# Optimization experiments

Hardware: AMD Instinct MI355X
Metric: run time of the kernel (lower is better)

The kernel has to match this reference:

```python
import jax, jax.numpy as jnp
import numpy as np

K = 16          # knn_graph k
FPS_RATIO = 0.5 # fps ratio
BN_EPS = 1e-5


def knn_idx(p, k):
    # p: [B, N, 3] -> neighbor indices [B, N, k] (loop=True: self included)
    n2 = jnp.sum(p * p, axis=-1)                                  # [B, N]
    d = n2[:, :, None] + n2[:, None, :] - 2.0 * jnp.einsum('bnc,bmc->bnm', p, p)
    _, idx = jax.lax.top_k(-d, k)                                 # smallest distances
    return idx


def gather_nbrs(x, idx):
    # x: [B, N, C], idx: [B, N, k] -> [B, N, k, C]
    return jax.vmap(lambda xb, ib: xb[ib])(x, idx)


def bn_silu(y, g, be):
    # training-mode BatchNorm over all rows (flattened) + SiLU, per PyG MLP defaults
    C = y.shape[-1]
    yf = y.reshape(-1, C)
    mu = jnp.mean(yf, axis=0)
    var = jnp.mean((yf - mu) ** 2, axis=0)
    return jax.nn.silu((y - mu) * jax.lax.rsqrt(var + BN_EPS) * g + be)


def fps_idx(p, m):
    # farthest point sampling on one cloud p: [N, 3], deterministic start at 0
    d0 = jnp.sum((p - p[0]) ** 2, axis=-1)
    def step(mind, _):
        i = jnp.argmax(mind)
        di = jnp.sum((p - p[i]) ** 2, axis=-1)
        return jnp.minimum(mind, di), i.astype(jnp.int32)
    _, idxs = jax.lax.scan(step, d0, None, length=m - 1)
    return jnp.concatenate([jnp.zeros((1,), jnp.int32), idxs])


def setup_inputs() -> dict:
    key = jax.random.key(0)
    ks = jax.random.split(key, 4)
    B, N, zdim = 16, 2048, 256
    return {
        'pos': jax.random.normal(ks[0], (B, N, 3), jnp.float32),
        'W1': jax.random.normal(ks[1], (6, 64), jnp.float32) * (1.0 / np.sqrt(6)),
        'b1': jnp.zeros((64,), jnp.float32),
        'g1': jnp.ones((64,), jnp.float32),
        'be1': jnp.zeros((64,), jnp.float32),
        'W2a': jax.random.normal(ks[2], (67, 128), jnp.float32) * (1.0 / np.sqrt(67)),
        'b2a': jnp.zeros((128,), jnp.float32),
        'g2a': jnp.ones((128,), jnp.float32),
        'be2a': jnp.zeros((128,), jnp.float32),
        'W2b': jax.random.normal(ks[3], (128, zdim), jnp.float32) * (1.0 / np.sqrt(128)),
        'b2b': jnp.zeros((zdim,), jnp.float32),
        'g2b': jnp.ones((zdim,), jnp.float32),
        'be2b': jnp.zeros((zdim,), jnp.float32),
    }


def reference(pos, W1, b1, g1, be1, W2a, b2a, g2a, be2a, W2b, b2b, g2b, be2b):
    B, N, _ = pos.shape
    M = int(N * FPS_RATIO)

    # conv1: knn graph on pos, message = MLP([x_j, pos_j - pos_i]), max-aggr
    idx1 = knn_idx(pos, K)                                  # [B, N, K]
    pos_j = gather_nbrs(pos, idx1)                          # [B, N, K, 3]
    msg = jnp.concatenate([pos_j, pos_j - pos[:, :, None, :]], axis=-1)  # [B,N,K,6]
    h = bn_silu(msg @ W1 + b1, g1, be1)                     # [B, N, K, 64]
    h = jnp.max(h, axis=2)                                  # [B, N, 64]

    # farthest point sampling, ratio 0.5
    idx_f = jax.vmap(fps_idx, in_axes=(0, None))(pos, M)    # [B, M]
    h = jax.vmap(lambda a, i: a[i])(h, idx_f)               # [B, M, 64]
    pos2 = jax.vmap(lambda a, i: a[i])(pos, idx_f)          # [B, M, 3]

    # conv2: knn on sampled points, message = MLP2([h_j, pos_j - pos_i]), max-aggr
    idx2 = knn_idx(pos2, K)                                 # [B, M, K]
    h_j = gather_nbrs(h, idx2)                              # [B, M, K, 64]
    p_j = gather_nbrs(pos2, idx2)                           # [B, M, K, 3]
    msg2 = jnp.concatenate([h_j, p_j - pos2[:, :, None, :]], axis=-1)  # [B,M,K,67]
    h2 = bn_silu(msg2 @ W2a + b2a, g2a, be2a)               # [B, M, K, 128]
    h2 = bn_silu(h2 @ W2b + b2b, g2b, be2b)                 # [B, M, K, zdim]
    h2 = jnp.max(h2, axis=2)                                # [B, M, zdim]

    # global max aggregation per cloud
    return jnp.max(h2, axis=1)                              # [B, zdim]
```

## Files before the change

### kernel.cpp

```cpp
#include <hip/hip_runtime.h>
#include <hip/hip_bf16.h>

#define NB 16
#define NN 2048
#define KNNK 16
#define MM 1024
#define RC1 (NB*NN*KNNK)
#define RC2 (NB*MM*KNNK)

typedef unsigned long long u64;
typedef __attribute__((ext_vector_type(8))) short short8;
typedef __attribute__((ext_vector_type(4))) float f32x4;

__device__ __forceinline__ float frn_mul(float a, float b){ return __fmul_rn(a,b); }
__device__ __forceinline__ float frn_add(float a, float b){ return __fadd_rn(a,b); }
__device__ __forceinline__ float frn_sub(float a, float b){ return __fsub_rn(a,b); }
__device__ __forceinline__ float silu_f(float x){ return x / (1.0f + __expf(-x)); }
__device__ __forceinline__ u64 umax64(u64 a, u64 b){ return a > b ? a : b; }

__device__ __forceinline__ unsigned f32_sortable(float f){
  unsigned u = __float_as_uint(f);
  return u ^ ((unsigned)((int)u >> 31) | 0x80000000u);
}
__device__ __forceinline__ unsigned short f2bf(float f){
  unsigned u = __float_as_uint(f);
  return (unsigned short)((u + 0x7FFFu + ((u >> 16) & 1u)) >> 16);
}
__device__ __forceinline__ float bf2f(unsigned short h){
  return __uint_as_float(((unsigned)h) << 16);
}

__device__ __forceinline__ void atomicMaxF(unsigned* addr, float v){
  if (v >= 0.f) atomicMax((int*)addr, (int)__float_as_uint(v));
  else          atomicMin(addr, __float_as_uint(v));
}
__device__ __forceinline__ void atomicMinF(unsigned* addr, float v){
  if (v >= 0.f) atomicMin((int*)addr, (int)__float_as_uint(v));
  else          atomicMax(addr, __float_as_uint(v));
}

__global__ __launch_bounds__(256) void init_kernel(float* stats1, float* stats2a, float* stats2b,
                                                   unsigned* gmax, unsigned* gmin){
  int t = blockIdx.x*256 + threadIdx.x;
  if (t < 128) stats1[t] = 0.f;
  if (t < 256) stats2a[t] = 0.f;
  if (t < 512) stats2b[t] = 0.f;
  if (t < 4096){ gmax[t] = 0xFF800000u; gmin[t] = 0x7F800000u; }
}

template<int CNT>
__device__ __forceinline__ void knn_scan(const float4* pts, int jbase,
                                         float xi, float yi, float zi, float n2i, u64* best){
#pragma unroll
  for (int p = 0; p < KNNK; ++p) best[p] = ~0ull;
  for (int jj = 0; jj < CNT; ++jj){
    float4 v = pts[jbase + jj];
    float e = frn_add(frn_add(frn_mul(xi,v.x), frn_mul(yi,v.y)), frn_mul(zi,v.z));
    float d = frn_sub(frn_add(n2i, v.w), frn_mul(2.0f, e));
    u64 key = ((u64)f32_sortable(d) << 32) | (unsigned)(jbase + jj);
    if (key < best[KNNK-1]){
      u64 cur = key;
#pragma unroll
      for (int p = 0; p < KNNK; ++p){
        u64 mn = best[p] < cur ? best[p] : cur;
        u64 mx = best[p] < cur ? cur : best[p];
        best[p] = mn; cur = mx;
      }
    }
  }
}

__global__ __launch_bounds__(256) void k0_fps_knn1(const float* __restrict__ pos,
    int* __restrict__ idxf, float* __restrict__ pos2, int* __restrict__ idx1,
    const float* __restrict__ W1, const float* __restrict__ b1, float* __restrict__ stats1){
  __shared__ __align__(16) char smem[77*1024];
  int tid = threadIdx.x;
  if (blockIdx.x < 16){
    int b = blockIdx.x;
    float4* pts4 = (float4*)smem;
    int* sel = (int*)(smem + 32*1024);
    u64* wred = (u64*)(smem + 36*1024);
    const float* pb = pos + (size_t)b*NN*3;
    float X[8], Y[8], Z[8], MD[8];
    unsigned LO[8];
#pragma unroll
    for (int q = 0; q < 8; ++q){
      int p = tid + 256*q;
      float x = pb[p*3+0], y = pb[p*3+1], z = pb[p*3+2];
      X[q] = x; Y[q] = y; Z[q] = z;
      LO[q] = ~(unsigned)p;
      pts4[p] = make_float4(x, y, z, 0.f);
    }
    float qx = pb[0], qy = pb[1], qz = pb[2];
#pragma unroll
    for (int q = 0; q < 8; ++q){
      float dx = frn_sub(X[q],qx), dy = frn_sub(Y[q],qy), dz = frn_sub(Z[q],qz);
      MD[q] = frn_add(frn_add(frn_mul(dx,dx), frn_mul(dy,dy)), frn_mul(dz,dz));
    }
    if (tid == 0) sel[0] = 0;
    int wv = tid >> 6;
    __syncthreads();
    for (int s = 1; s < MM; ++s){
      u64 t0 = umax64(((u64)__float_as_uint(MD[0])<<32)|LO[0], ((u64)__float_as_uint(MD[1])<<32)|LO[1]);
      u64 t1 = umax64(((u64)__float_as_uint(MD[2])<<32)|LO[2], ((u64)__float_as_uint(MD[3])<<32)|LO[3]);
      u64 t2 = umax64(((u64)__float_as_uint(MD[4])<<32)|LO[4], ((u64)__float_as_uint(MD[5])<<32)|LO[5]);
      u64 t3 = umax64(((u64)__float_as_uint(MD[6])<<32)|LO[6], ((u64)__float_as_uint(MD[7])<<32)|LO[7]);
      u64 kk = umax64(umax64(t0, t1), umax64(t2, t3));
#define RED_DPP(CTRL) { \
      unsigned lo_ = (unsigned)kk, hi_ = (unsigned)(kk>>32); \
      unsigned plo = (unsigned)__builtin_amdgcn_update_dpp((int)lo_,(int)lo_,CTRL,0xF,0xF,false); \
      unsigned phi = (unsigned)__builtin_amdgcn_update_dpp((int)hi_,(int)hi_,CTRL,0xF,0xF,false); \
      u64 o = ((u64)phi<<32)|plo; kk = o > kk ? o : kk; }
      RED_DPP(0xB1)
      RED_DPP(0x4E)
      RED_DPP(0x124)
      RED_DPP(0x128)
      RED_DPP(0x142)
      RED_DPP(0x143)
#undef RED_DPP
      int par = s & 1;
      if ((tid & 63) == 63) wred[par*4 + wv] = kk;
      __syncthreads();
      const u64* wr = wred + par*4;
      u64 K = umax64(umax64(wr[0], wr[1]), umax64(wr[2], wr[3]));
      unsigned wp = ~(unsigned)K;
      if (tid == 0) sel[s] = (int)wp;
      float4 wc = pts4[wp];
#pragma unroll
      for (int q = 0; q < 8; ++q){
        float dx = frn_sub(X[q],wc.x), dy = frn_sub(Y[q],wc.y), dz = frn_sub(Z[q],wc.z);
        float d = frn_add(frn_add(frn_mul(dx,dx), frn_mul(dy,dy)), frn_mul(dz,dz));
        MD[q] = fminf(MD[q], d);
      }
    }
    __syncthreads();
    for (int m = tid; m < MM; m += 256){
      int j = sel[m];
      idxf[b*MM + m] = j;
      float4 c = pts4[j];
      pos2[(size_t)(b*MM+m)*3+0] = c.x;
      pos2[(size_t)(b*MM+m)*3+1] = c.y;
      pos2[(size_t)(b*MM+m)*3+2] = c.z;
    }
  } else {
    int cid = blockIdx.x - 16;
    int b = cid >> 4;
    int rb16 = cid & 15;
    float4* pts4 = (float4*)smem;
    u64* cres = (u64*)(smem + 32*1024);
    int* idxl = (int*)(smem + 32*1024 + 34816);
    float* red = (float*)(smem + 32*1024 + 34816 + 8704);
    const float* pb = pos + (size_t)b*NN*3;
    for (int i = tid; i < NN; i += 256){
      float x = pb[i*3+0], y = pb[i*3+1], z = pb[i*3+2];
      float n2 = frn_add(frn_add(frn_mul(x,x), frn_mul(y,y)), frn_mul(z,z));
      pts4[i] = make_float4(x, y, z, n2);
    }
    __syncthreads();
    int lrow = tid & 127;
    int ch = tid >> 7;
    int i = rb16*128 + lrow;
    float4 qv = pts4[i];
    u64 best[KNNK];
    knn_scan<1024>(pts4, ch*1024, qv.x, qv.y, qv.z, qv.w, best);
#pragma unroll
    for (int p = 0; p < KNNK; ++p) cres[tid*17 + p] = best[p];
    __syncthreads();
    if (tid < 128){
      const u64* A = cres + tid*17;
      const u64* B = cres + (tid + 128)*17;
      int ia = 0, ib = 0;
      int* op = idx1 + ((size_t)(b*NN + rb16*128 + tid))*KNNK;
#pragma unroll
      for (int p = 0; p < KNNK; ++p){
        u64 ka = A[ia], kb = B[ib];
        int v;
        if (ka < kb){ v = (int)(unsigned)ka; ++ia; }
        else        { v = (int)(unsigned)kb; ++ib; }
        op[p] = v;
        idxl[tid*17 + p] = v;
      }
    }
    __syncthreads();
    int lane = tid & 63, wv = tid >> 6;
    float w[6];
#pragma unroll
    for (int f = 0; f < 6; ++f) w[f] = W1[f*64 + lane];
    float bias = b1[lane];
    float ssum = 0.f, ssq = 0.f;
    for (int r = 0; r < 32; ++r){
      int lr = wv*32 + r;
      float4 pi = pts4[rb16*128 + lr];
      const int* ip = idxl + lr*17;
#pragma unroll 4
      for (int k = 0; k < KNNK; ++k){
        int j = ip[k];
        float4 pj = pts4[j];
        float y = bias;
        y = fmaf(pj.x, w[0], y); y = fmaf(pj.y, w[1], y); y = fmaf(pj.z, w[2], y);
        y = fmaf(pj.x - pi.x, w[3], y); y = fmaf(pj.y - pi.y, w[4], y); y = fmaf(pj.z - pi.z, w[5], y);
        ssum += y; ssq = fmaf(y, y, ssq);
      }
    }
    red[(wv*64+lane)*2+0] = ssum; red[(wv*64+lane)*2+1] = ssq;
    __syncthreads();
    if (tid < 64){
      float s = red[(0*64+lane)*2]+red[(1*64+lane)*2]+red[(2*64+lane)*2]+red[(3*64+lane)*2];
      float q = red[(0*64+lane)*2+1]+red[(1*64+lane)*2+1]+red[(2*64+lane)*2+1]+red[(3*64+lane)*2+1];
      atomicAdd(&stats1[lane], s);
      atomicAdd(&stats1[64+lane], q);
    }
  }
}

__global__ __launch_bounds__(256) void k1_knn2_c1apply(
    const float* __restrict__ pos2, int* __restrict__ idx2,
    const float* __restrict__ pos, const int* __restrict__ idx1,
    const float* __restrict__ W1, const float* __restrict__ b1,
    const float* __restrict__ g1, const float* __restrict__ be1,
    const float* __restrict__ stats1, unsigned short* __restrict__ hbf){
  __shared__ __align__(16) char smem[48*1024];
  int tid = threadIdx.x;
  if (blockIdx.x < 256){
    int b = blockIdx.x >> 4;
    int rb = blockIdx.x & 15;
    float4* sm = (float4*)smem;
    u64* cres = (u64*)(smem + 16*1024);
    const float* pb = pos2 + (size_t)b*MM*3;
    for (int t = tid; t < MM; t += 256){
      float x = pb[t*3+0], y = pb[t*3+1], z = pb[t*3+2];
      float n2 = frn_add(frn_add(frn_mul(x,x), frn_mul(y,y)), frn_mul(z,z));
      sm[t] = make_float4(x, y, z, n2);
    }
    __syncthreads();
    int trow = tid & 63, ch = tid >> 6;
    int i = rb*64 + trow;
    float4 qv = sm[i];
    u64 best[KNNK];
    knn_scan<256>(sm, ch*256, qv.x, qv.y, qv.z, qv.w, best);
#pragma unroll
    for (int p = 0; p < KNNK; ++p) cres[tid*KNNK + p] = best[p];
    __syncthreads();
    if (tid < 64){
      const u64* L0 = cres + tid*KNNK;
      const u64* L1 = cres + (64 + tid)*KNNK;
      const u64* L2 = cres + (128 + tid)*KNNK;
      const u64* L3 = cres + (192 + tid)*KNNK;
      int o0=0, o1=0, o2=0, o3=0;
      int* op = idx2 + ((size_t)(b*MM + rb*64 + tid))*KNNK;
#pragma unroll
      for (int p = 0; p < KNNK; ++p){
        u64 k0 = L0[o0], k1 = L1[o1], k2 = L2[o2], k3 = L3[o3];
        u64 m01 = k0 < k1 ? k0 : k1;
        u64 m23 = k2 < k3 ? k2 : k3;
        u64 m = m01 < m23 ? m01 : m23;
        op[p] = (int)(unsigned)m;
        o0 += (m == k0); o1 += (m == k1); o2 += (m == k2); o3 += (m == k3);
      }
    }
  } else {
    int lane = tid & 63, wv = tid >> 6;
    int wave = (blockIdx.x - 256)*4 + wv;
    float w[6];
#pragma unroll
    for (int f = 0; f < 6; ++f) w[f] = W1[f*64 + lane];
    float bias = b1[lane];
    const float inv = 1.0f / (float)RC1;
    float mu = stats1[lane] * inv;
    float var = fmaxf(stats1[64+lane]*inv - mu*mu, 0.f);
    float sc = rsqrtf(var + 1e-5f) * g1[lane];
    float sh = be1[lane] - mu*sc;
    for (int r = 0; r < 8; ++r){
      int row = wave*8 + r;
      int b = row >> 11, ii = row & 2047;
      const float* pi = pos + ((size_t)(b*NN + ii))*3;
      float xi = pi[0], yi = pi[1], zi = pi[2];
      const int* ip = idx1 + (size_t)row * KNNK;
      float ymn = INFINITY, ymx = -INFINITY;
#pragma unroll 4
      for (int k = 0; k < KNNK; ++k){
        int j = ip[k];
        const float* pj = pos + ((size_t)(b*NN + j))*3;
        float xj = pj[0], yj = pj[1], zj = pj[2];
        float y = bias;
        y = fmaf(xj, w[0], y); y = fmaf(yj, w[1], y); y = fmaf(zj, w[2], y);
        y = fmaf(xj - xi, w[3], y); y = fmaf(yj - yi, w[4], y); y = fmaf(zj - zi, w[5], y);
        ymn = fminf(ymn, y); ymx = fmaxf(ymx, y);
      }
      hbf[((size_t)row << 6) + lane] = f2bf(fmaxf(silu_f(fmaf(ymx, sc, sh)), silu_f(fmaf(ymn, sc, sh))));
    }
  }
}

__global__ __launch_bounds__(256) void conv2a_kernel(
    const unsigned short* __restrict__ hbf, const int* __restrict__ idxf,
    const float* __restrict__ pos2, const int* __restrict__ idx2,
    const float* __restrict__ W2a, const float* __restrict__ b2a,
    float* __restrict__ stats2a, __hip_bfloat16* __restrict__ y2a){
  __shared__ __align__(16) unsigned short At[64*104];
  __shared__ __align__(16) unsigned short Wt[128*104];
  __shared__ int qs[64];
  int tid = threadIdx.x;
  int lane = tid & 63, wvi = tid >> 6;
  for (int i = tid; i < 96*128; i += 256){
    int k = i >> 7, c = i & 127;
    Wt[c*104 + k] = (k < 67) ? f2bf(W2a[k*128 + c]) : (unsigned short)0;
  }
  for (int i = tid; i < 64*104/2; i += 256) ((unsigned*)At)[i] = 0u;
  __syncthreads();
  int cb = wvi*32;
  short8 bfrag[2][3];
#pragma unroll
  for (int cf = 0; cf < 2; ++cf)
#pragma unroll
    for (int kf = 0; kf < 3; ++kf){
      int col = cb + cf*16 + (lane & 15);
      bfrag[cf][kf] = *(short8*)(Wt + col*104 + kf*32 + (lane>>4)*8);
    }
  float bb[2] = { b2a[cb + (lane & 15)], b2a[cb + 16 + (lane & 15)] };
  float ssum[2] = {0.f, 0.f}, ssq[2] = {0.f, 0.f};
  for (int t = 0; t < 4; ++t){
    int tbase = (blockIdx.x*4 + t)*64;
    if (t > 0) __syncthreads();
    if (tid < 64){
      int grow = tbase + tid;
      int b = grow >> 14;
      int m = (grow >> 4) & 1023;
      int j = idx2[grow];
      int q = idxf[b*MM + j];
      qs[tid] = b*NN + q;
      const float* pm = pos2 + ((size_t)(b*MM + m))*3;
      const float* pj = pos2 + ((size_t)(b*MM + j))*3;
      At[tid*104 + 64] = f2bf(pj[0]-pm[0]);
      At[tid*104 + 65] = f2bf(pj[1]-pm[1]);
      At[tid*104 + 66] = f2bf(pj[2]-pm[2]);
    }
    __syncthreads();
    {
      int r = tid & 63, ck = tid >> 6;
      const unsigned short* src = hbf + (size_t)qs[r]*64 + ck*16;
      short8 v0 = *(const short8*)(src);
      short8 v1 = *(const short8*)(src + 8);
      *(short8*)(At + r*104 + ck*16) = v0;
      *(short8*)(At + r*104 + ck*16 + 8) = v1;
    }
    __syncthreads();
#pragma unroll
    for (int rf = 0; rf < 4; ++rf){
      int r = rf*16 + (lane & 15);
      short8 af[3];
#pragma unroll
      for (int kf = 0; kf < 3; ++kf)
        af[kf] = *(short8*)(At + r*104 + kf*32 + (lane>>4)*8);
#pragma unroll
      for (int cf = 0; cf < 2; ++cf){
        f32x4 acc = {0.f,0.f,0.f,0.f};
#pragma unroll
        for (int kf = 0; kf < 3; ++kf)
          acc = __builtin_amdgcn_mfma_f32_16x16x32_bf16(af[kf], bfrag[cf][kf], acc, 0, 0, 0);
#pragma unroll
        for (int jj = 0; jj < 4; ++jj){
          int row = tbase + rf*16 + (lane>>4)*4 + jj;
          int col = cb + cf*16 + (lane & 15);
          float y = acc[jj] + bb[cf];
          ssum[cf] += y; ssq[cf] = fmaf(y, y, ssq[cf]);
          y2a[(size_t)row*128 + col] = __float2bfloat16(y);
        }
      }
    }
  }
#pragma unroll
  for (int cf = 0; cf < 2; ++cf){
#pragma unroll
    for (int off = 16; off <= 32; off += 16){
      ssum[cf] += __shfl_xor(ssum[cf], off);
      ssq[cf]  += __shfl_xor(ssq[cf],  off);
    }
  }
  if ((lane >> 4) == 0){
    atomicAdd(&stats2a[cb + lane], ssum[0]);
    atomicAdd(&stats2a[128 + cb + lane], ssq[0]);
    atomicAdd(&stats2a[cb + 16 + lane], ssum[1]);
    atomicAdd(&stats2a[128 + cb + 16 + lane], ssq[1]);
  }
}

__global__ __launch_bounds__(256) void conv2b_kernel(
    const __hip_bfloat16* __restrict__ y2a, const float* __restrict__ stats2a,
    const float* __restrict__ g2a, const float* __restrict__ be2a,
    const float* __restrict__ W2b, const float* __restrict__ b2b,
    float* __restrict__ stats2b, unsigned* __restrict__ gmax, unsigned* __restrict__ gmin){
  __shared__ __align__(16) char Albs[64*256];
  __shared__ __align__(16) char Btbs[64*256];
  __shared__ float sc2a[128], sh2a[128];
  int tid = threadIdx.x;
  int lane = tid & 63, wvi = tid >> 6;
  int ct = blockIdx.x & 3;
  int rb = blockIdx.x >> 2;
  int c0 = ct * 64;
  int batch = rb >> 5;
  if (tid < 128){
    const float inv = 1.0f / (float)RC2;
    float mu = stats2a[tid] * inv;
    float var = fmaxf(stats2a[128+tid]*inv - mu*mu, 0.f);
    float s = rsqrtf(var + 1e-5f) * g2a[tid];
    sc2a[tid] = s; sh2a[tid] = be2a[tid] - mu*s;
  }
  {
    int cc = tid & 63, u0 = tid >> 6;
#pragma unroll
    for (int i = 0; i < 4; ++i){
      int u = u0 + i*4;
      unsigned short hb[8];
#pragma unroll
      for (int e = 0; e < 8; ++e) hb[e] = f2bf(W2b[(size_t)(u*8+e)*256 + c0 + cc]);
      *(short8*)(Btbs + cc*256 + u*16) = *(short8*)hb;
    }
  }
  __syncthreads();
  short8 bfrag[4];
#pragma unroll
  for (int kb4 = 0; kb4 < 4; ++kb4){
    int col_local = wvi*16 + (lane & 15);
    bfrag[kb4] = *(short8*)(Btbs + col_local*256 + kb4*64 + (lane>>4)*16);
  }
  float bb = b2b[c0 + wvi*16 + (lane & 15)];
  float vmn = INFINITY, vmx = -INFINITY, ssum = 0.f, ssq = 0.f;
  const unsigned short* y2u = (const unsigned short*)y2a;
  int sr = tid & 63, su = tid >> 6;
  for (int tile = 0; tile < 8; ++tile){
    int row0 = rb*512 + tile*64;
    if (tile > 0) __syncthreads();
#pragma unroll
    for (int i = 0; i < 4; ++i){
      int u = su + i*4;
      short8 v = *(const short8*)(y2u + (size_t)(row0 + sr)*128 + u*8);
      unsigned short ha[8];
#pragma unroll
      for (int e = 0; e < 8; ++e){
        int k = u*8 + e;
        float f = bf2f((unsigned short)v[e]);
        ha[e] = f2bf(silu_f(fmaf(f, sc2a[k], sh2a[k])));
      }
      *(short8*)(Albs + sr*256 + ((u*16) ^ ((sr & 7) << 4))) = *(short8*)ha;
    }
    __syncthreads();
#pragma unroll
    for (int sl = 0; sl < 4; ++sl){
      f32x4 acc = {0.f, 0.f, 0.f, 0.f};
#pragma unroll
      for (int kb4 = 0; kb4 < 4; ++kb4){
        int r = sl*16 + (lane & 15);
        short8 afrag = *(short8*)(Albs + r*256 + ((kb4*64 + (lane>>4)*16) ^ ((r & 7) << 4)));
        acc = __builtin_amdgcn_mfma_f32_16x16x32_bf16(afrag, bfrag[kb4], acc, 0, 0, 0);
      }
#pragma unroll
      for (int j = 0; j < 4; ++j){
        float y = acc[j] + bb;
        vmn = fminf(vmn, y); vmx = fmaxf(vmx, y);
        ssum += y; ssq = fmaf(y, y, ssq);
      }
    }
  }
#pragma unroll
  for (int off = 16; off <= 32; off += 16){
    vmn  = fminf(vmn,  __shfl_xor(vmn,  off));
    vmx  = fmaxf(vmx,  __shfl_xor(vmx,  off));
    ssum = ssum + __shfl_xor(ssum, off);
    ssq  = ssq  + __shfl_xor(ssq,  off);
  }
  if ((lane >> 4) == 0){
    int c = c0 + wvi*16 + lane;
    atomicAdd(&stats2b[c], ssum);
    atomicAdd(&stats2b[256+c], ssq);
    atomicMaxF(&gmax[batch*256 + c], vmx);
    atomicMinF(&gmin[batch*256 + c], vmn);
  }
}

__global__ __launch_bounds__(256) void final_kernel(
    const float* __restrict__ stats2b, const unsigned* __restrict__ gmax,
    const unsigned* __restrict__ gmin, const float* __restrict__ g2b,
    const float* __restrict__ be2b, float* __restrict__ out){
  int t = blockIdx.x*256 + threadIdx.x;
  if (t >= NB*256) return;
  int c = t & 255;
  const float inv = 1.0f / (float)RC2;
  float mu = stats2b[c]*inv;
  float var = fmaxf(stats2b[256+c]*inv - mu*mu, 0.f);
  float sc = rsqrtf(var + 1e-5f)*g2b[c];
  float sh = be2b[c] - mu*sc;
  float mx = __uint_as_float(gmax[t]);
  float mn = __uint_as_float(gmin[t]);
  out[t] = fmaxf(silu_f(fmaf(mx, sc, sh)), silu_f(fmaf(mn, sc, sh)));
}

extern "C" void kernel_launch(void* const* d_in, const int* in_sizes, int n_in,
                              void* d_out, int out_size, void* d_ws, size_t ws_size,
                              hipStream_t stream){
  (void)in_sizes; (void)n_in; (void)out_size; (void)ws_size;
  const float* pos  = (const float*)d_in[0];
  const float* W1   = (const float*)d_in[1];
  const float* b1   = (const float*)d_in[2];
  const float* g1   = (const float*)d_in[3];
  const float* be1  = (const float*)d_in[4];
  const float* W2a  = (const float*)d_in[5];
  const float* b2a  = (const float*)d_in[6];
  const float* g2a  = (const float*)d_in[7];
  const float* be2a = (const float*)d_in[8];
  const float* W2b  = (const float*)d_in[9];
  const float* b2b  = (const float*)d_in[10];
  const float* g2b  = (const float*)d_in[11];
  const float* be2b = (const float*)d_in[12];

  char* w = (char*)d_ws;
  size_t off = 0;
  auto carve = [&](size_t bytes)->void*{ void* p = w + off; off += (bytes + 255) & ~(size_t)255; return p; };
  int*      idx1    = (int*)carve((size_t)NB*NN*KNNK*4);
  unsigned short* hbf = (unsigned short*)carve((size_t)NB*NN*64*2);
  int*      idxf    = (int*)carve((size_t)NB*MM*4);
  float*    pos2    = (float*)carve((size_t)NB*MM*3*4);
  int*      idx2    = (int*)carve((size_t)NB*MM*KNNK*4);
  float*    stats1  = (float*)carve(128*4);
  float*    stats2a = (float*)carve(256*4);
  float*    stats2b = (float*)carve(512*4);
  unsigned* gmax    = (unsigned*)carve(4096*4);
  unsigned* gmin    = (unsigned*)carve(4096*4);
  __hip_bfloat16* y2a = (__hip_bfloat16*)carve((size_t)RC2*128*2);

  init_kernel<<<dim3(16), dim3(256), 0, stream>>>(stats1, stats2a, stats2b, gmax, gmin);
  k0_fps_knn1<<<dim3(272), dim3(256), 0, stream>>>(pos, idxf, pos2, idx1, W1, b1, stats1);
  k1_knn2_c1apply<<<dim3(1280), dim3(256), 0, stream>>>(pos2, idx2, pos, idx1, W1, b1, g1, be1, stats1, hbf);
  conv2a_kernel<<<dim3(1024), dim3(256), 0, stream>>>(hbf, idxf, pos2, idx2, W2a, b2a, stats2a, y2a);
  conv2b_kernel<<<dim3(2048), dim3(256), 0, stream>>>(y2a, stats2a, g2a, be2a, W2b, b2b, stats2b, gmax, gmin);
  final_kernel<<<dim3(16), dim3(256), 0, stream>>>(stats2b, gmax, gmin, g2b, be2b, (float*)d_out);
}
```

Baseline: 825.1 us.

## Merge FPS/knn1 and knn2/conv1-apply into one kernel with spin-wait flags

```diff
diff --git a/kernel.cpp b/kernel.cpp
--- a/kernel.cpp
+++ b/kernel.cpp
@@ -40,12 +40,13 @@
 }
 
 __global__ __launch_bounds__(256) void init_kernel(float* stats1, float* stats2a, float* stats2b,
-                                                   unsigned* gmax, unsigned* gmin){
+                                                   unsigned* gmax, unsigned* gmin, unsigned* sync){
   int t = blockIdx.x*256 + threadIdx.x;
   if (t < 128) stats1[t] = 0.f;
   if (t < 256) stats2a[t] = 0.f;
   if (t < 512) stats2b[t] = 0.f;
   if (t < 4096){ gmax[t] = 0xFF800000u; gmin[t] = 0x7F800000u; }
+  if (t >= 4096 && t < 4160) sync[t - 4096] = 0u;
 }
 
 template<int CNT>
@@ -70,10 +71,12 @@
   }
 }
 
-__global__ __launch_bounds__(256) void k0_fps_knn1(const float* __restrict__ pos,
+__global__ __launch_bounds__(256) void k0_mega(const float* __restrict__ pos,
     int* __restrict__ idxf, float* __restrict__ pos2, int* __restrict__ idx1,
-    const float* __restrict__ W1, const float* __restrict__ b1, float* __restrict__ stats1){
-  __shared__ __align__(16) char smem[77*1024];
+    int* __restrict__ idx2, const float* __restrict__ W1, const float* __restrict__ b1,
+    const float* __restrict__ g1, const float* __restrict__ be1,
+    float* __restrict__ stats1, unsigned short* __restrict__ hbf, unsigned* sync){
+  __shared__ __align__(16) char smem[82*1024];
   int tid = threadIdx.x;
   if (blockIdx.x < 16){
     int b = blockIdx.x;
@@ -142,7 +145,10 @@
       pos2[(size_t)(b*MM+m)*3+1] = c.y;
       pos2[(size_t)(b*MM+m)*3+2] = c.z;
     }
-  } else {
+    __syncthreads();
+    __threadfence();
+    if (tid == 0) atomicExch(&sync[1 + b], 1u);
+  } else if (blockIdx.x < 272){
     int cid = blockIdx.x - 16;
     int b = cid >> 4;
     int rb16 = cid & 15;
@@ -210,57 +216,17 @@
       atomicAdd(&stats1[lane], s);
       atomicAdd(&stats1[64+lane], q);
     }
-  }
-}
-
-__global__ __launch_bounds__(256) void k1_knn2_c1apply(
-    const float* __restrict__ pos2, int* __restrict__ idx2,
-    const float* __restrict__ pos, const int* __restrict__ idx1,
-    const float* __restrict__ W1, const float* __restrict__ b1,
-    const float* __restrict__ g1, const float* __restrict__ be1,
-    const float* __restrict__ stats1, unsigned short* __restrict__ hbf){
-  __shared__ __align__(16) char smem[48*1024];
-  int tid = threadIdx.x;
-  if (blockIdx.x < 256){
-    int b = blockIdx.x >> 4;
-    int rb = blockIdx.x & 15;
-    float4* sm = (float4*)smem;
-    u64* cres = (u64*)(smem + 16*1024);
-    const float* pb = pos2 + (size_t)b*MM*3;
-    for (int t = tid; t < MM; t += 256){
-      float x = pb[t*3+0], y = pb[t*3+1], z = pb[t*3+2];
-      float n2 = frn_add(frn_add(frn_mul(x,x), frn_mul(y,y)), frn_mul(z,z));
-      sm[t] = make_float4(x, y, z, n2);
-    }
-    __syncthreads();
-    int trow = tid & 63, ch = tid >> 6;
-    int i = rb*64 + trow;
-    float4 qv = sm[i];
-    u64 best[KNNK];
-    knn_scan<256>(sm, ch*256, qv.x, qv.y, qv.z, qv.w, best);
-#pragma unroll
-    for (int p = 0; p < KNNK; ++p) cres[tid*KNNK + p] = best[p];
-    __syncthreads();
-    if (tid < 64){
-      const u64* L0 = cres + tid*KNNK;
-      const u64* L1 = cres + (64 + tid)*KNNK;
-      const u64* L2 = cres + (128 + tid)*KNNK;
-      const u64* L3 = cres + (192 + tid)*KNNK;
-      int o0=0, o1=0, o2=0, o3=0;
-      int* op = idx2 + ((size_t)(b*MM + rb*64 + tid))*KNNK;
-#pragma unroll
-      for (int p = 0; p < KNNK; ++p){
-        u64 k0 = L0[o0], k1 = L1[o1], k2 = L2[o2], k3 = L3[o3];
-        u64 m01 = k0 < k1 ? k0 : k1;
-        u64 m23 = k2 < k3 ? k2 : k3;
-        u64 m = m01 < m23 ? m01 : m23;
-        op[p] = (int)(unsigned)m;
-        o0 += (m == k0); o1 += (m == k1); o2 += (m == k2); o3 += (m == k3);
-      }
-    }
-  } else {
+    __syncthreads();
+    __threadfence();
+    if (tid == 0) atomicAdd(&sync[0], 1u);
+  } else if (blockIdx.x < 1296){
+    if (tid == 0){
+      while (atomicAdd(&sync[0], 0u) < 256u) __builtin_amdgcn_s_sleep(32);
+    }
+    __syncthreads();
+    __threadfence();
     int lane = tid & 63, wv = tid >> 6;
-    int wave = (blockIdx.x - 256)*4 + wv;
+    int wave = (blockIdx.x - 272)*4 + wv;
     float w[6];
 #pragma unroll
     for (int f = 0; f < 6; ++f) w[f] = W1[f*64 + lane];
@@ -289,6 +255,49 @@
       }
       hbf[((size_t)row << 6) + lane] = f2bf(fmaxf(silu_f(fmaf(ymx, sc, sh)), silu_f(fmaf(ymn, sc, sh))));
     }
+  } else {
+    int cid = blockIdx.x - 1296;
+    int b = cid >> 4;
+    int rb = cid & 15;
+    if (tid == 0){
+      while (atomicAdd(&sync[1 + b], 0u) == 0u) __builtin_amdgcn_s_sleep(32);
+    }
+    __syncthreads();
+    __threadfence();
+    float4* sm = (float4*)smem;
+    u64* cres = (u64*)(smem + 16*1024);
+    const float* pb = pos2 + (size_t)b*MM*3;
+    for (int t = tid; t < MM; t += 256){
+      float x = pb[t*3+0], y = pb[t*3+1], z = pb[t*3+2];
+      float n2 = frn_add(frn_add(frn_mul(x,x), frn_mul(y,y)), frn_mul(z,z));
+      sm[t] = make_float4(x, y, z, n2);
+    }
+    __syncthreads();
+    int trow = tid & 63, ch = tid >> 6;
+    int i = rb*64 + trow;
+    float4 qv = sm[i];
+    u64 best[KNNK];
+    knn_scan<256>(sm, ch*256, qv.x, qv.y, qv.z, qv.w, best);
+#pragma unroll
+    for (int p = 0; p < KNNK; ++p) cres[tid*KNNK + p] = best[p];
+    __syncthreads();
+    if (tid < 64){
+      const u64* L0 = cres + tid*KNNK;
+      const u64* L1 = cres + (64 + tid)*KNNK;
+      const u64* L2 = cres + (128 + tid)*KNNK;
+      const u64* L3 = cres + (192 + tid)*KNNK;
+      int o0=0, o1=0, o2=0, o3=0;
+      int* op = idx2 + ((size_t)(b*MM + rb*64 + tid))*KNNK;
+#pragma unroll
+      for (int p = 0; p < KNNK; ++p){
+        u64 k0 = L0[o0], k1 = L1[o1], k2 = L2[o2], k3 = L3[o3];
+        u64 m01 = k0 < k1 ? k0 : k1;
+        u64 m23 = k2 < k3 ? k2 : k3;
+        u64 m = m01 < m23 ? m01 : m23;
+        op[p] = (int)(unsigned)m;
+        o0 += (m == k0); o1 += (m == k1); o2 += (m == k2); o3 += (m == k3);
+      }
+    }
   }
 }
 
@@ -526,11 +535,12 @@
   float*    stats2b = (float*)carve(512*4);
   unsigned* gmax    = (unsigned*)carve(4096*4);
   unsigned* gmin    = (unsigned*)carve(4096*4);
+  unsigned* sync    = (unsigned*)carve(64*4);
   __hip_bfloat16* y2a = (__hip_bfloat16*)carve((size_t)RC2*128*2);
 
-  init_kernel<<<dim3(16), dim3(256), 0, stream>>>(stats1, stats2a, stats2b, gmax, gmin);
-  k0_fps_knn1<<<dim3(272), dim3(256), 0, stream>>>(pos, idxf, pos2, idx1, W1, b1, stats1);
-  k1_knn2_c1apply<<<dim3(1280), dim3(256), 0, stream>>>(pos2, idx2, pos, idx1, W1, b1, g1, be1, stats1, hbf);
+  init_kernel<<<dim3(17), dim3(256), 0, stream>>>(stats1, stats2a, stats2b, gmax, gmin, sync);
+  k0_mega<<<dim3(1552), dim3(256), 0, stream>>>(pos, idxf, pos2, idx1, idx2,
+                                                W1, b1, g1, be1, stats1, hbf, sync);
   conv2a_kernel<<<dim3(1024), dim3(256), 0, stream>>>(hbf, idxf, pos2, idx2, W2a, b2a, stats2a, y2a);
   conv2b_kernel<<<dim3(2048), dim3(256), 0, stream>>>(y2a, stats2a, g2a, be2a, W2b, b2b, stats2b, gmax, gmin);
   final_kernel<<<dim3(16), dim3(256), 0, stream>>>(stats2b, gmax, gmin, g2b, be2b, (float*)d_out);
```

Measured after the change: 1.521 ms. +84.3%, slower.

## Widen conv2b column tile to 128 and stage conv1 positions in LDS

Applied to the files above, without the earlier changes.

```diff
diff --git a/kernel.cpp b/kernel.cpp
--- a/kernel.cpp
+++ b/kernel.cpp
@@ -259,8 +259,15 @@
       }
     }
   } else {
+    float4* pts4 = (float4*)smem;
+    int bblk = blockIdx.x - 256;
+    int b = bblk >> 6;
+    const float* pb = pos + (size_t)b*NN*3;
+    for (int i = tid; i < NN; i += 256)
+      pts4[i] = make_float4(pb[i*3+0], pb[i*3+1], pb[i*3+2], 0.f);
+    __syncthreads();
     int lane = tid & 63, wv = tid >> 6;
-    int wave = (blockIdx.x - 256)*4 + wv;
+    int wave = bblk*4 + wv;
     float w[6];
 #pragma unroll
     for (int f = 0; f < 6; ++f) w[f] = W1[f*64 + lane];
@@ -272,19 +279,17 @@
     float sh = be1[lane] - mu*sc;
     for (int r = 0; r < 8; ++r){
       int row = wave*8 + r;
-      int b = row >> 11, ii = row & 2047;
-      const float* pi = pos + ((size_t)(b*NN + ii))*3;
-      float xi = pi[0], yi = pi[1], zi = pi[2];
+      int ii = row & 2047;
+      float4 pi = pts4[ii];
       const int* ip = idx1 + (size_t)row * KNNK;
       float ymn = INFINITY, ymx = -INFINITY;
 #pragma unroll 4
       for (int k = 0; k < KNNK; ++k){
         int j = ip[k];
-        const float* pj = pos + ((size_t)(b*NN + j))*3;
-        float xj = pj[0], yj = pj[1], zj = pj[2];
+        float4 pj = pts4[j];
         float y = bias;
-        y = fmaf(xj, w[0], y); y = fmaf(yj, w[1], y); y = fmaf(zj, w[2], y);
-        y = fmaf(xj - xi, w[3], y); y = fmaf(yj - yi, w[4], y); y = fmaf(zj - zi, w[5], y);
+        y = fmaf(pj.x, w[0], y); y = fmaf(pj.y, w[1], y); y = fmaf(pj.z, w[2], y);
+        y = fmaf(pj.x - pi.x, w[3], y); y = fmaf(pj.y - pi.y, w[4], y); y = fmaf(pj.z - pi.z, w[5], y);
         ymn = fminf(ymn, y); ymx = fmaxf(ymx, y);
       }
       hbf[((size_t)row << 6) + lane] = f2bf(fmaxf(silu_f(fmaf(ymx, sc, sh)), silu_f(fmaf(ymn, sc, sh))));
@@ -391,13 +396,13 @@
     const float* __restrict__ W2b, const float* __restrict__ b2b,
     float* __restrict__ stats2b, unsigned* __restrict__ gmax, unsigned* __restrict__ gmin){
   __shared__ __align__(16) char Albs[64*256];
-  __shared__ __align__(16) char Btbs[64*256];
+  __shared__ __align__(16) char Btbs[128*256];
   __shared__ float sc2a[128], sh2a[128];
   int tid = threadIdx.x;
   int lane = tid & 63, wvi = tid >> 6;
-  int ct = blockIdx.x & 3;
-  int rb = blockIdx.x >> 2;
-  int c0 = ct * 64;
+  int ct = blockIdx.x & 1;
+  int rb = blockIdx.x >> 1;
+  int c0 = ct * 128;
   int batch = rb >> 5;
   if (tid < 128){
     const float inv = 1.0f / (float)RC2;
@@ -407,10 +412,10 @@
     sc2a[tid] = s; sh2a[tid] = be2a[tid] - mu*s;
   }
   {
-    int cc = tid & 63, u0 = tid >> 6;
-#pragma unroll
-    for (int i = 0; i < 4; ++i){
-      int u = u0 + i*4;
+    int cc = tid & 127, u0 = tid >> 7;
+#pragma unroll
+    for (int i = 0; i < 8; ++i){
+      int u = u0 + i*2;
       unsigned short hb[8];
 #pragma unroll
       for (int e = 0; e < 8; ++e) hb[e] = f2bf(W2b[(size_t)(u*8+e)*256 + c0 + cc]);
@@ -418,14 +423,17 @@
     }
   }
   __syncthreads();
-  short8 bfrag[4];
-#pragma unroll
-  for (int kb4 = 0; kb4 < 4; ++kb4){
-    int col_local = wvi*16 + (lane & 15);
-    bfrag[kb4] = *(short8*)(Btbs + col_local*256 + kb4*64 + (lane>>4)*16);
-  }
-  float bb = b2b[c0 + wvi*16 + (lane & 15)];
-  float vmn = INFINITY, vmx = -INFINITY, ssum = 0.f, ssq = 0.f;
+  short8 bfrag[2][4];
+#pragma unroll
+  for (int cf = 0; cf < 2; ++cf)
+#pragma unroll
+    for (int kb4 = 0; kb4 < 4; ++kb4){
+      int col_local = wvi*32 + cf*16 + (lane & 15);
+      bfrag[cf][kb4] = *(short8*)(Btbs + col_local*256 + kb4*64 + (lane>>4)*16);
+    }
+  float bb[2] = { b2b[c0 + wvi*32 + (lane & 15)], b2b[c0 + wvi*32 + 16 + (lane & 15)] };
+  float vmn[2] = {INFINITY, INFINITY}, vmx[2] = {-INFINITY, -INFINITY};
+  float ssum[2] = {0.f, 0.f}, ssq[2] = {0.f, 0.f};
   const unsigned short* y2u = (const unsigned short*)y2a;
   int sr = tid & 63, su = tid >> 6;
   for (int tile = 0; tile < 8; ++tile){
@@ -447,34 +455,45 @@
     __syncthreads();
 #pragma unroll
     for (int sl = 0; sl < 4; ++sl){
-      f32x4 acc = {0.f, 0.f, 0.f, 0.f};
-#pragma unroll
-      for (int kb4 = 0; kb4 < 4; ++kb4){
-        int r = sl*16 + (lane & 15);
-        short8 afrag = *(short8*)(Albs + r*256 + ((kb4*64 + (lane>>4)*16) ^ ((r & 7) << 4)));
-        acc = __builtin_amdgcn_mfma_f32_16x16x32_bf16(afrag, bfrag[kb4], acc, 0, 0, 0);
-      }
-#pragma unroll
-      for (int j = 0; j < 4; ++j){
-        float y = acc[j] + bb;
-        vmn = fminf(vmn, y); vmx = fmaxf(vmx, y);
-        ssum += y; ssq = fmaf(y, y, ssq);
-      }
-    }
-  }
-#pragma unroll
-  for (int off = 16; off <= 32; off += 16){
-    vmn  = fminf(vmn,  __shfl_xor(vmn,  off));
-    vmx  = fmaxf(vmx,  __shfl_xor(vmx,  off));
-    ssum = ssum + __shfl_xor(ssum, off);
-    ssq  = ssq  + __shfl_xor(ssq,  off);
+      int r = sl*16 + (lane & 15);
+      short8 af[4];
+#pragma unroll
+      for (int kb4 = 0; kb4 < 4; ++kb4)
+        af[kb4] = *(short8*)(Albs + r*256 + ((kb4*64 + (lane>>4)*16) ^ ((r & 7) << 4)));
+#pragma unroll
+      for (int cf = 0; cf < 2; ++cf){
+        f32x4 acc = {0.f, 0.f, 0.f, 0.f};
+#pragma unroll
+        for (int kb4 = 0; kb4 < 4; ++kb4)
+          acc = __builtin_amdgcn_mfma_f32_16x16x32_bf16(af[kb4], bfrag[cf][kb4], acc, 0, 0, 0);
+#pragma unroll
+        for (int j = 0; j < 4; ++j){
+          float y = acc[j] + bb[cf];
+          vmn[cf] = fminf(vmn[cf], y); vmx[cf] = fmaxf(vmx[cf], y);
+          ssum[cf] += y; ssq[cf] = fmaf(y, y, ssq[cf]);
+        }
+      }
+    }
+  }
+#pragma unroll
+  for (int cf = 0; cf < 2; ++cf){
+#pragma unroll
+    for (int off = 16; off <= 32; off += 16){
+      vmn[cf]  = fminf(vmn[cf],  __shfl_xor(vmn[cf],  off));
+      vmx[cf]  = fmaxf(vmx[cf],  __shfl_xor(vmx[cf],  off));
+      ssum[cf] = ssum[cf] + __shfl_xor(ssum[cf], off);
+      ssq[cf]  = ssq[cf]  + __shfl_xor(ssq[cf],  off);
+    }
   }
   if ((lane >> 4) == 0){
-    int c = c0 + wvi*16 + lane;
-    atomicAdd(&stats2b[c], ssum);
-    atomicAdd(&stats2b[256+c], ssq);
-    atomicMaxF(&gmax[batch*256 + c], vmx);
-    atomicMinF(&gmin[batch*256 + c], vmn);
+#pragma unroll
+    for (int cf = 0; cf < 2; ++cf){
+      int c = c0 + wvi*32 + cf*16 + lane;
+      atomicAdd(&stats2b[c], ssum[cf]);
+      atomicAdd(&stats2b[256+c], ssq[cf]);
+      atomicMaxF(&gmax[batch*256 + c], vmx[cf]);
+      atomicMinF(&gmin[batch*256 + c], vmn[cf]);
+    }
   }
 }
 
@@ -532,6 +551,6 @@
   k0_fps_knn1<<<dim3(272), dim3(256), 0, stream>>>(pos, idxf, pos2, idx1, W1, b1, stats1);
   k1_knn2_c1apply<<<dim3(1280), dim3(256), 0, stream>>>(pos2, idx2, pos, idx1, W1, b1, g1, be1, stats1, hbf);
   conv2a_kernel<<<dim3(1024), dim3(256), 0, stream>>>(hbf, idxf, pos2, idx2, W2a, b2a, stats2a, y2a);
-  conv2b_kernel<<<dim3(2048), dim3(256), 0, stream>>>(y2a, stats2a, g2a, be2a, W2b, b2b, stats2b, gmax, gmin);
+  conv2b_kernel<<<dim3(1024), dim3(256), 0, stream>>>(y2a, stats2a, g2a, be2a, W2b, b2b, stats2b, gmax, gmin);
   final_kernel<<<dim3(16), dim3(256), 0, stream>>>(stats2b, gmax, gmin, g2b, be2b, (float*)d_out);
 }
```

Result: faster. 801.8 us (median of 2 runs) (-2.8%).
